# Kernel optimization log

Measured on AMD Instinct MI355X. Metric: run time of the kernel, lower is better.

The kernel has to match this reference:

```python
import jax, jax.numpy as jnp
import numpy as np

NUM_STAB = 0.001  # numerical_stabilizer from relu_kernel_transformation


def relu_kernel(data, proj):
    """ReLU random-feature kernel: data [B,L,H,D], proj [M,D] -> [B,L,H,M]."""
    ratio = 1.0 / jnp.sqrt(jnp.asarray(proj.shape[0], jnp.float32))
    data_dash = ratio * jnp.einsum('blhd,md->blhm', data, proj)
    return jax.nn.relu(data_dash) + NUM_STAB


def setup_inputs() -> dict:
    key = jax.random.key(0)
    k1, k2, k3, k4 = jax.random.split(key, 4)
    B, L, H, D, M = 2, 4096, 8, 64, 256
    return {
        'query': jax.random.normal(k1, (B, L, H, D), jnp.float32),
        'key_t': jax.random.normal(k2, (B, L, H, D), jnp.float32),
        'value': jax.random.normal(k3, (B, L, H, D), jnp.float32),
        'projection_matrix': jax.random.normal(k4, (M, D), jnp.float32),
    }


def reference(query, key_t, value, projection_matrix):
    # Kernel feature maps [B,L,H,M]
    qp = relu_kernel(query, projection_matrix)
    kp = relu_kernel(key_t, projection_matrix)
    # Causal path operates in [L,B,H,*] layout
    qs = jnp.transpose(qp, (1, 0, 2, 3))     # [L,B,H,M]
    ks = jnp.transpose(kp, (1, 0, 2, 3))     # [L,B,H,M]
    vs = jnp.transpose(value, (1, 0, 2, 3))  # [L,B,H,D]

    B, H, M = qs.shape[1], qs.shape[2], qs.shape[3]
    D = vs.shape[3]
    init = (jnp.zeros((B, H, M, D), qs.dtype),  # running sum of k outer v
            jnp.zeros((B, H, M), qs.dtype))     # running sum of k

    def step(carry, inp):
        kv_sum, k_sum = carry
        q, k, v = inp  # [B,H,M], [B,H,M], [B,H,D]
        kv_sum = kv_sum + k[..., None] * v[..., None, :]
        k_sum = k_sum + k
        num = jnp.einsum('bhmd,bhm->bhd', kv_sum, q)  # causal numerator step
        den = jnp.einsum('bhm,bhm->bh', q, k_sum)     # causal denominator step
        return (kv_sum, k_sum), (num, den)

    _, (num, den) = jax.lax.scan(step, init, (qs, ks, vs))  # num [L,B,H,D], den [L,B,H]
    den = den[..., None]
    den = jnp.where(den <= 0.0, jnp.ones_like(den), den)
    out = num / den                      # [L,B,H,D]
    return jnp.transpose(out, (1, 0, 2, 3))  # [B,L,H,D]
```

## Files before the change

kernel.cpp:

```cpp
#include <hip/hip_runtime.h>
#include <hip/hip_bf16.h>


#define B_   2
#define L_   4096
#define H_   8
#define D_   64
#define M_   256
#define T_   128
#define C_   (L_ / T_)
#define NBH  (B_ * H_)
#define RATIO 0.0625f
#define STAB  0.001f
#define SVT  136
#define SQS  72

typedef __attribute__((ext_vector_type(8))) short short8;
typedef __attribute__((ext_vector_type(4))) float floatx4;

#define MFMA16(a, b, c) __builtin_amdgcn_mfma_f32_16x16x32_bf16(a, b, c, 0, 0, 0)

__device__ inline unsigned short f2bf(float x) {
    union { float f; unsigned u; } v; v.f = x;
    unsigned r = v.u + 0x7FFF + ((v.u >> 16) & 1);
    return (unsigned short)(r >> 16);
}
__device__ inline unsigned pack2bf(float a, float b) {
    __hip_bfloat162 h = __float22bfloat162_rn(make_float2(a, b));
    unsigned u; __builtin_memcpy(&u, &h, 4);
    return u;
}
__device__ inline short8 ldg8_bfs(const float* p) {
    float4 a = *(const float4*)p;
    float4 b = *(const float4*)(p + 4);
    short8 r;
    r[0] = (short)f2bf(a.x * RATIO); r[1] = (short)f2bf(a.y * RATIO);
    r[2] = (short)f2bf(a.z * RATIO); r[3] = (short)f2bf(a.w * RATIO);
    r[4] = (short)f2bf(b.x * RATIO); r[5] = (short)f2bf(b.y * RATIO);
    r[6] = (short)f2bf(b.z * RATIO); r[7] = (short)f2bf(b.w * RATIO);
    return r;
}
__device__ inline short8 ldg8_bf(const float* p) {
    float4 a = *(const float4*)p;
    float4 b = *(const float4*)(p + 4);
    short8 r;
    r[0] = (short)f2bf(a.x); r[1] = (short)f2bf(a.y);
    r[2] = (short)f2bf(a.z); r[3] = (short)f2bf(a.w);
    r[4] = (short)f2bf(b.x); r[5] = (short)f2bf(b.y);
    r[6] = (short)f2bf(b.z); r[7] = (short)f2bf(b.w);
    return r;
}

__global__ __launch_bounds__(512, 2)
void chunk_kernel(const float* __restrict__ key, const float* __restrict__ val,
                  const float* __restrict__ proj,
                  unsigned short* __restrict__ VTg, unsigned short* __restrict__ Pbf,
                  float* __restrict__ Ppart, float* __restrict__ Zpart) {
    const int c = blockIdx.x, bh = blockIdx.y;
    const int b = bh / H_, h = bh % H_;
    const int tid = threadIdx.x;
    const int w = tid >> 6, lane = tid & 63;
    const int l15 = lane & 15, quad = lane >> 4;

    __shared__ __align__(16) unsigned short VT[64 * SVT];
    __shared__ __align__(16) unsigned short KpT[128 * SVT];
    __shared__ __align__(16) unsigned short KbfL[T_ * D_];

    const size_t rowstr = H_ * D_;
    const size_t base = ((size_t)b * L_ + (size_t)c * T_) * rowstr + (size_t)h * D_;

    for (int i = tid; i < T_ * 8; i += 512) {
        int t = i >> 3, d8 = (i & 7) * 8;
        short8 kv = ldg8_bfs(key + base + (size_t)t * rowstr + d8);
        int rt = t >> 4, l = t & 15, kk = d8 >> 5, q = (d8 & 31) >> 3;
        *(short8*)&KbfL[((rt * 2 + kk) * 64 + q * 16 + l) << 3] = kv;
    }
    for (int i = tid; i < T_ * 16; i += 512) {
        int t = i >> 4, d4 = (i & 15) * 4;
        float4 vv = *(const float4*)(val + base + (size_t)t * rowstr + d4);
        VT[(d4 + 0) * SVT + t] = f2bf(vv.x);
        VT[(d4 + 1) * SVT + t] = f2bf(vv.y);
        VT[(d4 + 2) * SVT + t] = f2bf(vv.z);
        VT[(d4 + 3) * SVT + t] = f2bf(vv.w);
    }
    __syncthreads();
    unsigned short* vout = VTg + ((size_t)bh * C_ + c) * (D_ * T_);
    for (int i = tid; i < D_ * 16; i += 512) {
        int d = i >> 4, tt = (i & 15) * 8;
        *(uint4*)(vout + d * T_ + tt) = *(const uint4*)&VT[d * SVT + tt];
    }
    if (c == 0 && tid < 256) {
        int i = bh * 256 + tid;
        float4 pv = *(const float4*)(proj + (size_t)i * 4);
        uint2 o; o.x = pack2bf(pv.x, pv.y); o.y = pack2bf(pv.z, pv.w);
        *(uint2*)(Pbf + (size_t)i * 4) = o;
    }

    float* Pp = Ppart + ((size_t)bh * C_ + c) * (D_ * M_);

    for (int half = 0; half < 2; ++half) {
        const int mrow = half * 128 + w * 16 + l15;
        short8 pf0 = ldg8_bf(proj + (size_t)mrow * D_ + quad * 8);
        short8 pf1 = ldg8_bf(proj + (size_t)mrow * D_ + 32 + quad * 8);
        if (half) __syncthreads();
        float zp = 0.f;
#pragma unroll
        for (int rt = 0; rt < 8; ++rt) {
            short8 kf0 = *(const short8*)&KbfL[((rt * 2 + 0) * 64 + lane) << 3];
            short8 kf1 = *(const short8*)&KbfL[((rt * 2 + 1) * 64 + lane) << 3];
            floatx4 a = {0.f, 0.f, 0.f, 0.f};
            a = MFMA16(kf0, pf0, a);
            a = MFMA16(kf1, pf1, a);
            float k0 = fmaxf(a[0], 0.f) + STAB;
            float k1 = fmaxf(a[1], 0.f) + STAB;
            float k2 = fmaxf(a[2], 0.f) + STAB;
            float k3 = fmaxf(a[3], 0.f) + STAB;
            zp += (k0 + k1) + (k2 + k3);
            uint2 pk; pk.x = pack2bf(k0, k1); pk.y = pack2bf(k2, k3);
            *(uint2*)&KpT[(w * 16 + l15) * SVT + rt * 16 + quad * 4] = pk;
        }
        zp += __shfl_xor(zp, 16, 64);
        zp += __shfl_xor(zp, 32, 64);
        if (quad == 0)
            Zpart[((size_t)bh * C_ + c) * M_ + mrow] = zp;
        __syncthreads();

        const int dt_w = w >> 1;
        const int mt0 = (w & 1) * 4;
        short8 vf[4];
#pragma unroll
        for (int k4 = 0; k4 < 4; ++k4)
            vf[k4] = *(const short8*)&VT[(dt_w * 16 + l15) * SVT + k4 * 32 + quad * 8];
#pragma unroll
        for (int mt = 0; mt < 4; ++mt) {
            floatx4 acc = {0.f, 0.f, 0.f, 0.f};
#pragma unroll
            for (int k4 = 0; k4 < 4; ++k4) {
                short8 kb = *(const short8*)&KpT[((mt0 + mt) * 16 + l15) * SVT
                                                 + k4 * 32 + quad * 8];
                acc = MFMA16(vf[k4], kb, acc);
            }
            const int mcol = half * 128 + (mt0 + mt) * 16 + l15;
#pragma unroll
            for (int r = 0; r < 4; ++r)
                Pp[(size_t)(dt_w * 16 + quad * 4 + r) * M_ + mcol] = acc[r];
        }
    }
}

__global__ __launch_bounds__(256, 4)
void prefix_kernel(const float* __restrict__ Ppart, const float* __restrict__ Zpart,
                   unsigned short* __restrict__ S, float* __restrict__ Z) {
    const int g = blockIdx.x, bh = blockIdx.y;
    const int tid = threadIdx.x;
    if (g < 16) {
        const size_t dm = ((size_t)g * 256 + tid) * 4;
        const float* Pp = Ppart + (size_t)bh * C_ * (D_ * M_) + dm;
        unsigned short* Sp = S + (size_t)bh * C_ * (D_ * M_) + dm;
        float4 acc = make_float4(0.f, 0.f, 0.f, 0.f);
#pragma unroll 8
        for (int c = 0; c < C_; ++c) {
            float4 p = *(const float4*)(Pp + (size_t)c * (D_ * M_));
            uint2 o; o.x = pack2bf(acc.x, acc.y); o.y = pack2bf(acc.z, acc.w);
            *(uint2*)(Sp + (size_t)c * (D_ * M_)) = o;
            acc.x += p.x; acc.y += p.y; acc.z += p.z; acc.w += p.w;
        }
    } else {
        const float* Zp = Zpart + (size_t)bh * C_ * M_ + tid;
        float* Zo = Z + (size_t)bh * C_ * M_ + tid;
        float acc = 0.f;
#pragma unroll 8
        for (int c = 0; c < C_; ++c) {
            float z = Zp[(size_t)c * M_];
            Zo[(size_t)c * M_] = acc;
            acc += z;
        }
    }
}

__global__ __launch_bounds__(512, 2)
void phase3_kernel(const float* __restrict__ q, const float* __restrict__ key,
                   const unsigned short* __restrict__ VTg,
                   const unsigned short* __restrict__ Pbf,
                   const unsigned short* __restrict__ S, const float* __restrict__ Z,
                   float* __restrict__ out) {
    const int c = blockIdx.x, bh = blockIdx.y;
    const int b = bh / H_, h = bh % H_;
    const int tid = threadIdx.x;
    const int w = tid >> 6, lane = tid & 63;
    const int l15 = lane & 15, quad = lane >> 4;

    __shared__ __align__(16) unsigned short KpL[T_ * SVT];
    __shared__ __align__(16) unsigned short QpS[8 * 16 * SQS];

    const size_t rowstr = H_ * D_;
    const size_t base = ((size_t)b * L_ + (size_t)c * T_) * rowstr + (size_t)h * D_;
    const unsigned short* Sp = S + (size_t)(bh * C_ + c) * (M_ * D_);
    const float* Zp = Z + (size_t)(bh * C_ + c) * M_;
    const unsigned short* Vc = VTg + ((size_t)bh * C_ + c) * (D_ * T_);

    short8 qf[2], kf[2];
#pragma unroll
    for (int kk = 0; kk < 2; ++kk) {
        size_t ro = base + (size_t)(16 * w + l15) * rowstr + kk * 32 + quad * 8;
        qf[kk] = ldg8_bfs(q + ro);
        kf[kk] = ldg8_bfs(key + ro);
    }

    unsigned short* myQp = QpS + w * 16 * SQS;
    floatx4 num[4];
    floatx4 Aacc[8];
#pragma unroll
    for (int dt = 0; dt < 4; ++dt) { floatx4 z4 = {0.f,0.f,0.f,0.f}; num[dt] = z4; }
#pragma unroll
    for (int ct = 0; ct < 8; ++ct) { floatx4 z4 = {0.f,0.f,0.f,0.f}; Aacc[ct] = z4; }
    float dz[4] = {0.f, 0.f, 0.f, 0.f};

    for (int hh = 0; hh < 2; ++hh) {
        short8 qa[4];
#pragma unroll
        for (int fgl = 0; fgl < 2; ++fgl) {
            const int fg = 2 * hh + fgl;
#pragma unroll
            for (int ct = 0; ct < 4; ++ct) {
                const unsigned short* pp = Pbf + (size_t)(fg * 64 + ct * 16 + l15) * D_;
                short8 pf0 = *(const short8*)(pp + quad * 8);
                short8 pf1 = *(const short8*)(pp + 32 + quad * 8);
                floatx4 aq = {0.f, 0.f, 0.f, 0.f};
                aq = MFMA16(qf[0], pf0, aq);
                aq = MFMA16(qf[1], pf1, aq);
                floatx4 ak = {0.f, 0.f, 0.f, 0.f};
                ak = MFMA16(kf[0], pf0, ak);
                ak = MFMA16(kf[1], pf1, ak);
                const int mloc = fgl * 64 + ct * 16 + l15;
                float zv = Zp[hh * 128 + mloc];
#pragma unroll
                for (int r = 0; r < 4; ++r) {
                    float qpv = fmaxf(aq[r], 0.f) + STAB;
                    float kpv = fmaxf(ak[r], 0.f) + STAB;
                    myQp[(quad * 4 + r) * SQS + ct * 16 + l15] = f2bf(qpv);
                    KpL[(size_t)(16 * w + quad * 4 + r) * SVT + mloc] = f2bf(kpv);
                    dz[r] = fmaf(qpv, zv, dz[r]);
                }
            }
#pragma unroll
            for (int kk = 0; kk < 2; ++kk)
                qa[fgl * 2 + kk] = *(const short8*)&myQp[l15 * SQS + kk * 32 + quad * 8];
        }
#pragma unroll
        for (int dt = 0; dt < 4; ++dt)
#pragma unroll
            for (int kc = 0; kc < 4; ++kc) {
                short8 sb = *(const short8*)(Sp + (size_t)(dt * 16 + l15) * M_
                                             + hh * 128 + kc * 32 + quad * 8);
                num[dt] = MFMA16(qa[kc], sb, num[dt]);
            }
        __syncthreads();
#pragma unroll
        for (int ct = 0; ct < 8; ++ct) {
            if (ct <= w) {
#pragma unroll
                for (int kc = 0; kc < 4; ++kc) {
                    short8 kb = *(const short8*)&KpL[(size_t)(ct * 16 + l15) * SVT
                                                     + kc * 32 + quad * 8];
                    Aacc[ct] = MFMA16(qa[kc], kb, Aacc[ct]);
                }
            }
        }
        __syncthreads();
    }
#pragma unroll
    for (int r = 0; r < 4; ++r) {
        dz[r] += __shfl_xor(dz[r], 1, 64);
        dz[r] += __shfl_xor(dz[r], 2, 64);
        dz[r] += __shfl_xor(dz[r], 4, 64);
        dz[r] += __shfl_xor(dz[r], 8, 64);
    }

    unsigned short* AmL = KpL;
    float da[4] = {0.f, 0.f, 0.f, 0.f};
#pragma unroll
    for (int ct = 0; ct < 8; ++ct)
#pragma unroll
        for (int r = 0; r < 4; ++r) {
            float av = Aacc[ct][r];
            if (ct > w || (ct == w && l15 > quad * 4 + r)) av = 0.f;
            AmL[(size_t)(16 * w + quad * 4 + r) * SVT + ct * 16 + l15] = f2bf(av);
            da[r] += av;
        }
#pragma unroll
    for (int r = 0; r < 4; ++r) {
        da[r] += __shfl_xor(da[r], 1, 64);
        da[r] += __shfl_xor(da[r], 2, 64);
        da[r] += __shfl_xor(da[r], 4, 64);
        da[r] += __shfl_xor(da[r], 8, 64);
    }

    for (int k4 = 0; k4 <= (w >> 1); ++k4) {
        short8 am = *(const short8*)&AmL[(size_t)(16 * w + l15) * SVT
                                         + k4 * 32 + quad * 8];
#pragma unroll
        for (int dt = 0; dt < 4; ++dt) {
            short8 vb = *(const short8*)(Vc + (size_t)(dt * 16 + l15) * T_
                                         + k4 * 32 + quad * 8);
            num[dt] = MFMA16(am, vb, num[dt]);
        }
    }

#pragma unroll
    for (int r = 0; r < 4; ++r) {
        float den = da[r] + dz[r];
        if (den <= 0.f) den = 1.f;
        float inv = 1.f / den;
        int t = 16 * w + quad * 4 + r;
#pragma unroll
        for (int dt = 0; dt < 4; ++dt)
            out[base + (size_t)t * rowstr + dt * 16 + l15] = num[dt][r] * inv;
    }
}

extern "C" void kernel_launch(void* const* d_in, const int* in_sizes, int n_in,
                              void* d_out, int out_size, void* d_ws, size_t ws_size,
                              hipStream_t stream) {
    const float* q    = (const float*)d_in[0];
    const float* k    = (const float*)d_in[1];
    const float* v    = (const float*)d_in[2];
    const float* proj = (const float*)d_in[3];
    float* out = (float*)d_out;

    const size_t nS = (size_t)NBH * C_ * D_ * M_;
    const size_t nZ = (size_t)NBH * C_ * M_;
    const size_t nV = (size_t)NBH * C_ * D_ * T_;
    unsigned short* S     = (unsigned short*)d_ws;
    float*          Z     = (float*)(S + nS);
    unsigned short* VTg   = (unsigned short*)(Z + nZ);
    unsigned short* Pbf   = VTg + nV;
    float*          Ppart = (float*)(Pbf + (size_t)M_ * D_);
    float*          Zpart = Ppart + nS;

    chunk_kernel<<<dim3(C_, NBH), dim3(512), 0, stream>>>(k, v, proj, VTg, Pbf, Ppart, Zpart);
    prefix_kernel<<<dim3(17, NBH), dim3(256), 0, stream>>>(Ppart, Zpart, S, Z);
    phase3_kernel<<<dim3(C_, NBH), dim3(512), 0, stream>>>(q, k, VTg, Pbf, S, Z, out);
}
```

Before: 158.0 us.

## Store key features in chunk kernel and split phase3 into single-wave blocks

The chunk kernel now also writes the bf16 ReLU key feature map for each chunk to a global workspace buffer, using strided 2-byte scattered stores. Phase3 no longer recomputes key features from raw keys. It reads them from that buffer instead and runs one 64-thread wave per 16-row slice, launched as 8x more blocks. This removes the duplicated key-projection MFMAs and the block-wide barriers, and lets the waves of a chunk be scheduled on their own. The costs are extra global traffic, redundant global reads of key features across waves, and poorly coalesced scattered writes.

```diff
diff --git a/kernel.cpp b/kernel.cpp
--- a/kernel.cpp
+++ b/kernel.cpp
@@ -55,7 +55,8 @@
 void chunk_kernel(const float* __restrict__ key, const float* __restrict__ val,
                   const float* __restrict__ proj,
                   unsigned short* __restrict__ VTg, unsigned short* __restrict__ Pbf,
-                  float* __restrict__ Ppart, float* __restrict__ Zpart) {
+                  float* __restrict__ Ppart, float* __restrict__ Zpart,
+                  unsigned short* __restrict__ KpG) {
     const int c = blockIdx.x, bh = blockIdx.y;
     const int b = bh / H_, h = bh % H_;
     const int tid = threadIdx.x;
@@ -102,6 +103,7 @@
         const int mrow = half * 128 + w * 16 + l15;
         short8 pf0 = ldg8_bf(proj + (size_t)mrow * D_ + quad * 8);
         short8 pf1 = ldg8_bf(proj + (size_t)mrow * D_ + 32 + quad * 8);
+        unsigned short* kgp = KpG + ((size_t)(bh * C_ + c)) * ((size_t)T_ * M_) + mrow;
         if (half) __syncthreads();
         float zp = 0.f;
 #pragma unroll
@@ -118,6 +120,11 @@
             zp += (k0 + k1) + (k2 + k3);
             uint2 pk; pk.x = pack2bf(k0, k1); pk.y = pack2bf(k2, k3);
             *(uint2*)&KpT[(w * 16 + l15) * SVT + rt * 16 + quad * 4] = pk;
+            const int t0 = rt * 16 + quad * 4;
+            kgp[(size_t)(t0 + 0) * M_] = (unsigned short)pk.x;
+            kgp[(size_t)(t0 + 1) * M_] = (unsigned short)(pk.x >> 16);
+            kgp[(size_t)(t0 + 2) * M_] = (unsigned short)pk.y;
+            kgp[(size_t)(t0 + 3) * M_] = (unsigned short)(pk.y >> 16);
         }
         zp += __shfl_xor(zp, 16, 64);
         zp += __shfl_xor(zp, 32, 64);
@@ -178,36 +185,33 @@
     }
 }
 
-__global__ __launch_bounds__(512, 2)
-void phase3_kernel(const float* __restrict__ q, const float* __restrict__ key,
+__global__ __launch_bounds__(64, 4)
+void phase3_kernel(const float* __restrict__ q,
                    const unsigned short* __restrict__ VTg,
                    const unsigned short* __restrict__ Pbf,
                    const unsigned short* __restrict__ S, const float* __restrict__ Z,
+                   const unsigned short* __restrict__ KpG,
                    float* __restrict__ out) {
-    const int c = blockIdx.x, bh = blockIdx.y;
+    const int c = blockIdx.x, bh = blockIdx.y, w = blockIdx.z;
     const int b = bh / H_, h = bh % H_;
-    const int tid = threadIdx.x;
-    const int w = tid >> 6, lane = tid & 63;
+    const int lane = threadIdx.x & 63;
     const int l15 = lane & 15, quad = lane >> 4;
 
-    __shared__ __align__(16) unsigned short KpL[T_ * SVT];
-    __shared__ __align__(16) unsigned short QpS[8 * 16 * SQS];
+    __shared__ __align__(16) unsigned short QpS[16 * SQS];
+    __shared__ __align__(16) unsigned short AmL[16 * SVT];
 
     const size_t rowstr = H_ * D_;
     const size_t base = ((size_t)b * L_ + (size_t)c * T_) * rowstr + (size_t)h * D_;
     const unsigned short* Sp = S + (size_t)(bh * C_ + c) * (M_ * D_);
     const float* Zp = Z + (size_t)(bh * C_ + c) * M_;
     const unsigned short* Vc = VTg + ((size_t)bh * C_ + c) * (D_ * T_);
-
-    short8 qf[2], kf[2];
-#pragma unroll
-    for (int kk = 0; kk < 2; ++kk) {
-        size_t ro = base + (size_t)(16 * w + l15) * rowstr + kk * 32 + quad * 8;
-        qf[kk] = ldg8_bfs(q + ro);
-        kf[kk] = ldg8_bfs(key + ro);
-    }
-
-    unsigned short* myQp = QpS + w * 16 * SQS;
+    const unsigned short* Kc = KpG + ((size_t)(bh * C_ + c)) * ((size_t)T_ * M_);
+
+    short8 qf[2];
+#pragma unroll
+    for (int kk = 0; kk < 2; ++kk)
+        qf[kk] = ldg8_bfs(q + base + (size_t)(16 * w + l15) * rowstr + kk * 32 + quad * 8);
+
     floatx4 num[4];
     floatx4 Aacc[8];
 #pragma unroll
@@ -229,23 +233,18 @@
                 floatx4 aq = {0.f, 0.f, 0.f, 0.f};
                 aq = MFMA16(qf[0], pf0, aq);
                 aq = MFMA16(qf[1], pf1, aq);
-                floatx4 ak = {0.f, 0.f, 0.f, 0.f};
-                ak = MFMA16(kf[0], pf0, ak);
-                ak = MFMA16(kf[1], pf1, ak);
                 const int mloc = fgl * 64 + ct * 16 + l15;
                 float zv = Zp[hh * 128 + mloc];
 #pragma unroll
                 for (int r = 0; r < 4; ++r) {
                     float qpv = fmaxf(aq[r], 0.f) + STAB;
-                    float kpv = fmaxf(ak[r], 0.f) + STAB;
-                    myQp[(quad * 4 + r) * SQS + ct * 16 + l15] = f2bf(qpv);
-                    KpL[(size_t)(16 * w + quad * 4 + r) * SVT + mloc] = f2bf(kpv);
+                    QpS[(quad * 4 + r) * SQS + ct * 16 + l15] = f2bf(qpv);
                     dz[r] = fmaf(qpv, zv, dz[r]);
                 }
             }
 #pragma unroll
             for (int kk = 0; kk < 2; ++kk)
-                qa[fgl * 2 + kk] = *(const short8*)&myQp[l15 * SQS + kk * 32 + quad * 8];
+                qa[fgl * 2 + kk] = *(const short8*)&QpS[l15 * SQS + kk * 32 + quad * 8];
         }
 #pragma unroll
         for (int dt = 0; dt < 4; ++dt)
@@ -255,19 +254,17 @@
                                              + hh * 128 + kc * 32 + quad * 8);
                 num[dt] = MFMA16(qa[kc], sb, num[dt]);
             }
-        __syncthreads();
 #pragma unroll
         for (int ct = 0; ct < 8; ++ct) {
             if (ct <= w) {
 #pragma unroll
                 for (int kc = 0; kc < 4; ++kc) {
-                    short8 kb = *(const short8*)&KpL[(size_t)(ct * 16 + l15) * SVT
-                                                     + kc * 32 + quad * 8];
+                    short8 kb = *(const short8*)(Kc + (size_t)(ct * 16 + l15) * M_
+                                                 + hh * 128 + kc * 32 + quad * 8);
                     Aacc[ct] = MFMA16(qa[kc], kb, Aacc[ct]);
                 }
             }
         }
-        __syncthreads();
     }
 #pragma unroll
     for (int r = 0; r < 4; ++r) {
@@ -277,7 +274,6 @@
         dz[r] += __shfl_xor(dz[r], 8, 64);
     }
 
-    unsigned short* AmL = KpL;
     float da[4] = {0.f, 0.f, 0.f, 0.f};
 #pragma unroll
     for (int ct = 0; ct < 8; ++ct)
@@ -285,7 +281,7 @@
         for (int r = 0; r < 4; ++r) {
             float av = Aacc[ct][r];
             if (ct > w || (ct == w && l15 > quad * 4 + r)) av = 0.f;
-            AmL[(size_t)(16 * w + quad * 4 + r) * SVT + ct * 16 + l15] = f2bf(av);
+            AmL[(quad * 4 + r) * SVT + ct * 16 + l15] = f2bf(av);
             da[r] += av;
         }
 #pragma unroll
@@ -297,8 +293,7 @@
     }
 
     for (int k4 = 0; k4 <= (w >> 1); ++k4) {
-        short8 am = *(const short8*)&AmL[(size_t)(16 * w + l15) * SVT
-                                         + k4 * 32 + quad * 8];
+        short8 am = *(const short8*)&AmL[l15 * SVT + k4 * 32 + quad * 8];
 #pragma unroll
         for (int dt = 0; dt < 4; ++dt) {
             short8 vb = *(const short8*)(Vc + (size_t)(dt * 16 + l15) * T_
@@ -331,14 +326,16 @@
     const size_t nS = (size_t)NBH * C_ * D_ * M_;
     const size_t nZ = (size_t)NBH * C_ * M_;
     const size_t nV = (size_t)NBH * C_ * D_ * T_;
+    const size_t nK = (size_t)NBH * C_ * T_ * M_;
     unsigned short* S     = (unsigned short*)d_ws;
     float*          Z     = (float*)(S + nS);
     unsigned short* VTg   = (unsigned short*)(Z + nZ);
     unsigned short* Pbf   = VTg + nV;
     float*          Ppart = (float*)(Pbf + (size_t)M_ * D_);
     float*          Zpart = Ppart + nS;
-
-    chunk_kernel<<<dim3(C_, NBH), dim3(512), 0, stream>>>(k, v, proj, VTg, Pbf, Ppart, Zpart);
+    unsigned short* KpG   = (unsigned short*)(Zpart + nZ);
+
+    chunk_kernel<<<dim3(C_, NBH), dim3(512), 0, stream>>>(k, v, proj, VTg, Pbf, Ppart, Zpart, KpG);
     prefix_kernel<<<dim3(17, NBH), dim3(256), 0, stream>>>(Ppart, Zpart, S, Z);
-    phase3_kernel<<<dim3(C_, NBH), dim3(512), 0, stream>>>(q, k, VTg, Pbf, S, Z, out);
-}
+    phase3_kernel<<<dim3(C_, NBH, 8), dim3(64), 0, stream>>>(q, VTg, Pbf, S, Z, KpG, out);
+}
```

New measurement: 181.4 us. +14.9%, slower.
